# Performance work log

Hardware: AMD Instinct MI355X
Metric: run time of the kernel (lower is better)

## Reference

```python
import jax, jax.numpy as jnp
import numpy as np

B, S, D = 2, 2048, 256
H, C = 8, 32          # headNum, cDim (D == H*C)
OUT = 256             # outDim
WIN = 32              # localWindowSize (half-width)
NEG = -1e30


def setup_inputs() -> dict:
    key = jax.random.key(0)
    ks = jax.random.split(key, 9)
    scale_qk = 1.0 / np.sqrt(D)
    return {
        "Qin": jax.random.normal(ks[0], (B, S, D), jnp.float32),
        "Kin": jax.random.normal(ks[1], (B, S, D), jnp.float32),
        "Vin": jax.random.normal(ks[2], (B, S, D), jnp.float32),
        "QTrans": jax.random.normal(ks[3], (D, H * C), jnp.float32) * scale_qk,
        "KTrans": jax.random.normal(ks[4], (D, H * C), jnp.float32) * scale_qk,
        "VTrans": jax.random.normal(ks[5], (D, H * C), jnp.float32) * scale_qk,
        "GW": jax.random.normal(ks[6], (H * C, D), jnp.float32) * scale_qk,  # nn.Linear weight [out,in]
        "Gb": jnp.ones((H * C,), jnp.float32),
        "OW": jax.random.normal(ks[7], (OUT, H * C), jnp.float32) * scale_qk,
        "Ob": jnp.zeros((OUT,), jnp.float32),
    }


def reference(Qin, Kin, Vin, QTrans, KTrans, VTrans, GW, Gb, OW, Ob):
    b, s, _ = Qin.shape
    # projections -> [b, s, H, C]
    Q = (Qin @ QTrans).reshape(b, s, H, C)
    K = (Kin @ KTrans).reshape(b, s, H, C)
    V = (Vin @ VTrans).reshape(b, s, H, C)
    G = jax.nn.sigmoid(Vin @ GW.T + Gb).reshape(b, s, H, C)

    # dense scores [b, H, s, t] (matches original hnst layout with batch/head swapped)
    A = jnp.einsum('bshc,bthc->bhst', Q, K) / jnp.sqrt(jnp.asarray(C, Q.dtype))

    # whose index clamping only re-hits in-window edge positions)
    idx = jnp.arange(s)
    local = jnp.abs(idx[:, None] - idx[None, :]) <= WIN  # [s, s]
    A = jnp.where(local[None, None, :, :], A, NEG)

    A = jax.nn.softmax(A, axis=-1)

    # gated attention output: original einsum 'hnst,hnti,hnsi->nshi'
    O = jnp.einsum('bhst,bthc,bshc->bshc', A, V, G)
    return O.reshape(b, s, H * C) @ OW.T + Ob
```

## Files before the change

### kernel.cpp

```cpp
#include <hip/hip_runtime.h>
#include <hip/hip_bf16.h>

typedef __bf16 bf16_t;
typedef __attribute__((ext_vector_type(8))) __bf16 bf16x8;
typedef __attribute__((ext_vector_type(4))) __bf16 bf16x4;
typedef __attribute__((ext_vector_type(4))) float f32x4;

#define MFMA(a, b, c) __builtin_amdgcn_mfma_f32_16x16x32_bf16((a), (b), (c), 0, 0, 0)

static __device__ __forceinline__ bf16x8 zero_bf16x8() {
  bf16x8 z;
#pragma unroll
  for (int i = 0; i < 8; ++i) z[i] = (bf16_t)0.f;
  return z;
}

__global__ __launch_bounds__(256) void prep_weights(
    const float* __restrict__ QT, const float* __restrict__ KT,
    const float* __restrict__ VTr, const float* __restrict__ GW,
    const float* __restrict__ OW, bf16_t* __restrict__ Wb) {
  int e = blockIdx.x * 256 + threadIdx.x;
  int mat = e >> 16;
  int r = e & 65535;
  const float* src = (mat == 0) ? QT : (mat == 1) ? KT : (mat == 2) ? VTr
                     : (mat == 3) ? GW : OW;
  float v = src[r];
  int dst;
  if (mat < 3) {
    int k = r >> 8, n = r & 255;
    dst = n * 256 + k;
  } else {
    dst = r;
  }
  Wb[mat * 65536 + dst] = (bf16_t)v;
}

__global__ __launch_bounds__(256) void proj_kernel(
    const float* __restrict__ Qin, const float* __restrict__ Kin,
    const float* __restrict__ Vin, const bf16_t* __restrict__ Wb,
    const float* __restrict__ Gb, bf16_t* __restrict__ Qb,
    bf16_t* __restrict__ Kb, bf16_t* __restrict__ VT, bf16_t* __restrict__ G) {
  const int tid = threadIdx.x, w = tid >> 6, lane = tid & 63;
  const int quad = lane >> 4, t15 = lane & 15;
  const int job = blockIdx.z;
  const int m0 = blockIdx.x * 64 + w * 16;
  const int n0 = blockIdx.y * 64;
  const float* A = (job == 0) ? Qin : (job == 1) ? Kin : Vin;
  const bf16_t* W = Wb + job * 65536;

  const f32x4 zf = {0.f, 0.f, 0.f, 0.f};
  f32x4 acc[4] = {zf, zf, zf, zf};

  for (int kc = 0; kc < 8; ++kc) {
    const float* ap = A + (size_t)(m0 + t15) * 256 + kc * 32 + quad * 8;
    float4 x0 = *(const float4*)ap;
    float4 x1 = *(const float4*)(ap + 4);
    bf16x8 a;
    a[0] = (bf16_t)x0.x; a[1] = (bf16_t)x0.y; a[2] = (bf16_t)x0.z; a[3] = (bf16_t)x0.w;
    a[4] = (bf16_t)x1.x; a[5] = (bf16_t)x1.y; a[6] = (bf16_t)x1.z; a[7] = (bf16_t)x1.w;
#pragma unroll
    for (int nf = 0; nf < 4; ++nf) {
      bf16x8 bw = *(const bf16x8*)(W + (size_t)(n0 + nf * 16 + t15) * 256 + kc * 32 + quad * 8);
      acc[nf] = MFMA(a, bw, acc[nf]);
    }
  }

  const int mm0 = m0 + quad * 4;
  if (job == 2) {
    const int b = mm0 >> 11;
    const int s = mm0 & 2047;
#pragma unroll
    for (int nf = 0; nf < 4; ++nf) {
      int nn = n0 + nf * 16 + t15;
      int h = nn >> 5, c = nn & 31;
      bf16x4 v4;
#pragma unroll
      for (int r = 0; r < 4; ++r) v4[r] = (bf16_t)acc[nf][r];
      *(bf16x4*)(VT + (size_t)((b * 8 + h) * 32 + c) * 2048 + s) = v4;
    }
  } else if (job == 3) {
#pragma unroll
    for (int nf = 0; nf < 4; ++nf) {
      int nn = n0 + nf * 16 + t15;
      float bias = Gb[nn];
#pragma unroll
      for (int r = 0; r < 4; ++r) {
        float g = 1.f / (1.f + __expf(-(acc[nf][r] + bias)));
        G[(size_t)(mm0 + r) * 256 + nn] = (bf16_t)g;
      }
    }
  } else {
    bf16_t* dst = (job == 0) ? Qb : Kb;
#pragma unroll
    for (int nf = 0; nf < 4; ++nf) {
      int nn = n0 + nf * 16 + t15;
#pragma unroll
      for (int r = 0; r < 4; ++r)
        dst[(size_t)(mm0 + r) * 256 + nn] = (bf16_t)acc[nf][r];
    }
  }
}

__global__ __launch_bounds__(256) void attn_kernel(
    const bf16_t* __restrict__ Qb, const bf16_t* __restrict__ Kb,
    const bf16_t* __restrict__ VT, const bf16_t* __restrict__ G,
    bf16_t* __restrict__ O) {
  __shared__ bf16_t P[4][16][104];
  const int tid = threadIdx.x, w = tid >> 6, lane = tid & 63;
  const int quad = lane >> 4, t15 = lane & 15;
  const int unit = blockIdx.x * 4 + w;
  const int qt = unit & 127, bh = unit >> 7;
  const int h = bh & 7, b = bh >> 3;
  const int q0 = qt * 16, tbase = q0 - 32;
  const size_t rowbase = (size_t)b * 2048;

  bf16x8 aq = *(const bf16x8*)(Qb + (rowbase + q0 + t15) * 256 + h * 32 + quad * 8);

  const f32x4 zf = {0.f, 0.f, 0.f, 0.f};
  f32x4 sc[5];
#pragma unroll
  for (int j = 0; j < 5; ++j) {
    int t = tbase + j * 16 + t15;
    bf16x8 bk = zero_bf16x8();
    if ((unsigned)t < 2048u)
      bk = *(const bf16x8*)(Kb + (rowbase + t) * 256 + h * 32 + quad * 8);
    sc[j] = MFMA(aq, bk, zf);
  }

  const float scale = 0.17677669529663687f;
  float mx[4] = {-3.0e38f, -3.0e38f, -3.0e38f, -3.0e38f};
#pragma unroll
  for (int j = 0; j < 5; ++j) {
    int t = tbase + j * 16 + t15;
#pragma unroll
    for (int r = 0; r < 4; ++r) {
      int q = q0 + quad * 4 + r;
      int dd = q - t;
      bool valid = ((unsigned)t < 2048u) && (dd <= 32) && (dd >= -32);
      float v = valid ? sc[j][r] * scale : -1e30f;
      sc[j][r] = v;
      mx[r] = fmaxf(mx[r], v);
    }
  }
#pragma unroll
  for (int off = 1; off < 16; off <<= 1) {
#pragma unroll
    for (int r = 0; r < 4; ++r) mx[r] = fmaxf(mx[r], __shfl_xor(mx[r], off));
  }
  float sum[4] = {0.f, 0.f, 0.f, 0.f};
#pragma unroll
  for (int j = 0; j < 5; ++j) {
#pragma unroll
    for (int r = 0; r < 4; ++r) {
      float e = __expf(sc[j][r] - mx[r]);
      sc[j][r] = e;
      sum[r] += e;
    }
  }
#pragma unroll
  for (int off = 1; off < 16; off <<= 1) {
#pragma unroll
    for (int r = 0; r < 4; ++r) sum[r] += __shfl_xor(sum[r], off);
  }
  float inv[4];
#pragma unroll
  for (int r = 0; r < 4; ++r) inv[r] = 1.f / sum[r];

#pragma unroll
  for (int j = 0; j < 5; ++j) {
#pragma unroll
    for (int r = 0; r < 4; ++r)
      P[w][quad * 4 + r][j * 16 + t15] = (bf16_t)(sc[j][r] * inv[r]);
  }
#pragma unroll
  for (int r = 0; r < 4; ++r) P[w][quad * 4 + r][80 + t15] = (bf16_t)0.f;
  __syncthreads();

  f32x4 y0 = zf, y1 = zf;
#pragma unroll
  for (int kc = 0; kc < 3; ++kc) {
    bf16x8 pa = *(const bf16x8*)&P[w][t15][kc * 32 + quad * 8];
    int ts = tbase + kc * 32 + quad * 8;
    bf16x8 bv0 = zero_bf16x8(), bv1 = zero_bf16x8();
    if (ts >= 0 && ts + 8 <= 2048) {
      const bf16_t* vbase = VT + ((size_t)((b * 8 + h) * 32) + t15) * 2048 + ts;
      bv0 = *(const bf16x8*)vbase;
      bv1 = *(const bf16x8*)(vbase + (size_t)16 * 2048);
    }
    y0 = MFMA(pa, bv0, y0);
    y1 = MFMA(pa, bv1, y1);
  }

#pragma unroll
  for (int r = 0; r < 4; ++r) {
    int q = q0 + quad * 4 + r;
    size_t base = (rowbase + q) * 256 + h * 32;
    float g0 = (float)G[base + t15];
    float g1 = (float)G[base + 16 + t15];
    O[base + t15] = (bf16_t)(y0[r] * g0);
    O[base + 16 + t15] = (bf16_t)(y1[r] * g1);
  }
}

__global__ __launch_bounds__(256) void out_kernel(
    const bf16_t* __restrict__ O, const bf16_t* __restrict__ OWb,
    const float* __restrict__ Ob, float* __restrict__ out) {
  const int tid = threadIdx.x, w = tid >> 6, lane = tid & 63;
  const int quad = lane >> 4, t15 = lane & 15;
  const int m0 = blockIdx.x * 64 + w * 16;
  const int n0 = blockIdx.y * 64;

  const f32x4 zf = {0.f, 0.f, 0.f, 0.f};
  f32x4 acc[4] = {zf, zf, zf, zf};

  for (int kc = 0; kc < 8; ++kc) {
    bf16x8 a = *(const bf16x8*)(O + (size_t)(m0 + t15) * 256 + kc * 32 + quad * 8);
#pragma unroll
    for (int nf = 0; nf < 4; ++nf) {
      bf16x8 bw = *(const bf16x8*)(OWb + (size_t)(n0 + nf * 16 + t15) * 256 + kc * 32 + quad * 8);
      acc[nf] = MFMA(a, bw, acc[nf]);
    }
  }

  const int mm0 = m0 + quad * 4;
#pragma unroll
  for (int nf = 0; nf < 4; ++nf) {
    int nn = n0 + nf * 16 + t15;
    float bias = Ob[nn];
#pragma unroll
    for (int r = 0; r < 4; ++r)
      out[(size_t)(mm0 + r) * 256 + nn] = acc[nf][r] + bias;
  }
}

extern "C" void kernel_launch(void* const* d_in, const int* in_sizes, int n_in,
                              void* d_out, int out_size, void* d_ws, size_t ws_size,
                              hipStream_t stream) {
  const float* Qin = (const float*)d_in[0];
  const float* Kin = (const float*)d_in[1];
  const float* Vin = (const float*)d_in[2];
  const float* QT  = (const float*)d_in[3];
  const float* KT  = (const float*)d_in[4];
  const float* VTr = (const float*)d_in[5];
  const float* GW  = (const float*)d_in[6];
  const float* Gb  = (const float*)d_in[7];
  const float* OW  = (const float*)d_in[8];
  const float* Ob  = (const float*)d_in[9];
  float* out = (float*)d_out;

  char* ws = (char*)d_ws;
  const size_t MB = 1u << 20;
  bf16_t* Qb = (bf16_t*)(ws + 0 * MB);
  bf16_t* Kb = (bf16_t*)(ws + 2 * MB);
  bf16_t* VT = (bf16_t*)(ws + 4 * MB);
  bf16_t* G  = (bf16_t*)(ws + 6 * MB);
  bf16_t* O  = (bf16_t*)(ws + 8 * MB);
  bf16_t* Wb = (bf16_t*)(ws + 10 * MB);

  prep_weights<<<1280, 256, 0, stream>>>(QT, KT, VTr, GW, OW, Wb);
  proj_kernel<<<dim3(64, 4, 4), 256, 0, stream>>>(Qin, Kin, Vin, Wb, Gb, Qb, Kb, VT, G);
  attn_kernel<<<512, 256, 0, stream>>>(Qb, Kb, VT, G, O);
  out_kernel<<<dim3(64, 4), 256, 0, stream>>>(O, Wb + 4 * 65536, Ob, out);
}
```

Before: 116.7 us.

## Fuse weight conversion into projection and output projection into attention

Drops the separate weight-prep kernel. The projection kernel now converts its fp32 weight tile to bf16 directly into shared memory, transposing where needed. The attention kernel is widened so one 512-thread block covers all 8 heads of a 16-row query tile, keeps the gated output in LDS, and applies the output projection in place. This removes two launches and the global round trip of O and the bf16 weights, at the cost of redundant fp32 weight reads and conversion in every block and only 256 blocks for the fused attention stage.

```diff
diff --git a/kernel.cpp b/kernel.cpp
--- a/kernel.cpp
+++ b/kernel.cpp
@@ -8,6 +8,8 @@
 
 #define MFMA(a, b, c) __builtin_amdgcn_mfma_f32_16x16x32_bf16((a), (b), (c), 0, 0, 0)
 
+#define WK 260
+
 static __device__ __forceinline__ bf16x8 zero_bf16x8() {
   bf16x8 z;
 #pragma unroll
@@ -15,38 +17,63 @@
   return z;
 }
 
-__global__ __launch_bounds__(256) void prep_weights(
-    const float* __restrict__ QT, const float* __restrict__ KT,
-    const float* __restrict__ VTr, const float* __restrict__ GW,
-    const float* __restrict__ OW, bf16_t* __restrict__ Wb) {
-  int e = blockIdx.x * 256 + threadIdx.x;
-  int mat = e >> 16;
-  int r = e & 65535;
-  const float* src = (mat == 0) ? QT : (mat == 1) ? KT : (mat == 2) ? VTr
-                     : (mat == 3) ? GW : OW;
-  float v = src[r];
-  int dst;
-  if (mat < 3) {
-    int k = r >> 8, n = r & 255;
-    dst = n * 256 + k;
-  } else {
-    dst = r;
-  }
-  Wb[mat * 65536 + dst] = (bf16_t)v;
+static __device__ __forceinline__ bf16x8 join8(bf16x4 lo, bf16x4 hi) {
+  bf16x8 r;
+  r[0] = lo[0]; r[1] = lo[1]; r[2] = lo[2]; r[3] = lo[3];
+  r[4] = hi[0]; r[5] = hi[1]; r[6] = hi[2]; r[7] = hi[3];
+  return r;
+}
+
+static __device__ __forceinline__ bf16x8 cvt8(float4 a, float4 b) {
+  bf16x8 r;
+  r[0] = (bf16_t)a.x; r[1] = (bf16_t)a.y; r[2] = (bf16_t)a.z; r[3] = (bf16_t)a.w;
+  r[4] = (bf16_t)b.x; r[5] = (bf16_t)b.y; r[6] = (bf16_t)b.z; r[7] = (bf16_t)b.w;
+  return r;
 }
 
 __global__ __launch_bounds__(256) void proj_kernel(
     const float* __restrict__ Qin, const float* __restrict__ Kin,
-    const float* __restrict__ Vin, const bf16_t* __restrict__ Wb,
-    const float* __restrict__ Gb, bf16_t* __restrict__ Qb,
-    bf16_t* __restrict__ Kb, bf16_t* __restrict__ VT, bf16_t* __restrict__ G) {
+    const float* __restrict__ Vin, const float* __restrict__ QT,
+    const float* __restrict__ KT, const float* __restrict__ VTr,
+    const float* __restrict__ GW, const float* __restrict__ Gb,
+    bf16_t* __restrict__ Qb, bf16_t* __restrict__ Kb,
+    bf16_t* __restrict__ VT, bf16_t* __restrict__ G) {
+  __shared__ bf16_t Wl[64][WK];
   const int tid = threadIdx.x, w = tid >> 6, lane = tid & 63;
   const int quad = lane >> 4, t15 = lane & 15;
   const int job = blockIdx.z;
   const int m0 = blockIdx.x * 64 + w * 16;
   const int n0 = blockIdx.y * 64;
   const float* A = (job == 0) ? Qin : (job == 1) ? Kin : Vin;
-  const bf16_t* W = Wb + job * 65536;
+
+  if (job < 3) {
+    const float* src = (job == 0) ? QT : (job == 1) ? KT : VTr;
+    const int nl = tid & 63;
+    const int kq = (tid >> 6) * 4;
+#pragma unroll
+    for (int i = 0; i < 16; ++i) {
+      int k0 = i * 16 + kq;
+      float f0 = src[(size_t)(k0 + 0) * 256 + n0 + nl];
+      float f1 = src[(size_t)(k0 + 1) * 256 + n0 + nl];
+      float f2 = src[(size_t)(k0 + 2) * 256 + n0 + nl];
+      float f3 = src[(size_t)(k0 + 3) * 256 + n0 + nl];
+      bf16x4 w4;
+      w4[0] = (bf16_t)f0; w4[1] = (bf16_t)f1; w4[2] = (bf16_t)f2; w4[3] = (bf16_t)f3;
+      *(bf16x4*)&Wl[nl][k0] = w4;
+    }
+  } else {
+    const int kk = (tid & 63) * 4;
+    const int nw = tid >> 6;
+#pragma unroll
+    for (int i = 0; i < 16; ++i) {
+      int n = i * 4 + nw;
+      float4 v = *(const float4*)(GW + (size_t)(n0 + n) * 256 + kk);
+      bf16x4 w4;
+      w4[0] = (bf16_t)v.x; w4[1] = (bf16_t)v.y; w4[2] = (bf16_t)v.z; w4[3] = (bf16_t)v.w;
+      *(bf16x4*)&Wl[n][kk] = w4;
+    }
+  }
+  __syncthreads();
 
   const f32x4 zf = {0.f, 0.f, 0.f, 0.f};
   f32x4 acc[4] = {zf, zf, zf, zf};
@@ -55,13 +82,12 @@
     const float* ap = A + (size_t)(m0 + t15) * 256 + kc * 32 + quad * 8;
     float4 x0 = *(const float4*)ap;
     float4 x1 = *(const float4*)(ap + 4);
-    bf16x8 a;
-    a[0] = (bf16_t)x0.x; a[1] = (bf16_t)x0.y; a[2] = (bf16_t)x0.z; a[3] = (bf16_t)x0.w;
-    a[4] = (bf16_t)x1.x; a[5] = (bf16_t)x1.y; a[6] = (bf16_t)x1.z; a[7] = (bf16_t)x1.w;
-#pragma unroll
-    for (int nf = 0; nf < 4; ++nf) {
-      bf16x8 bw = *(const bf16x8*)(W + (size_t)(n0 + nf * 16 + t15) * 256 + kc * 32 + quad * 8);
-      acc[nf] = MFMA(a, bw, acc[nf]);
+    bf16x8 a = cvt8(x0, x1);
+#pragma unroll
+    for (int nf = 0; nf < 4; ++nf) {
+      bf16x4 lo = *(const bf16x4*)&Wl[nf * 16 + t15][kc * 32 + quad * 8];
+      bf16x4 hi = *(const bf16x4*)&Wl[nf * 16 + t15][kc * 32 + quad * 8 + 4];
+      acc[nf] = MFMA(a, join8(lo, hi), acc[nf]);
     }
   }
 
@@ -101,16 +127,16 @@
   }
 }
 
-__global__ __launch_bounds__(256) void attn_kernel(
+__global__ __launch_bounds__(512) void attn_out_kernel(
     const bf16_t* __restrict__ Qb, const bf16_t* __restrict__ Kb,
     const bf16_t* __restrict__ VT, const bf16_t* __restrict__ G,
-    bf16_t* __restrict__ O) {
-  __shared__ bf16_t P[4][16][104];
-  const int tid = threadIdx.x, w = tid >> 6, lane = tid & 63;
+    const float* __restrict__ OW, const float* __restrict__ Ob,
+    float* __restrict__ out) {
+  __shared__ bf16_t P[8][16][104];
+  __shared__ bf16_t Ol[16][WK];
+  const int tid = threadIdx.x, h = tid >> 6, lane = tid & 63;
   const int quad = lane >> 4, t15 = lane & 15;
-  const int unit = blockIdx.x * 4 + w;
-  const int qt = unit & 127, bh = unit >> 7;
-  const int h = bh & 7, b = bh >> 3;
+  const int qt = blockIdx.x & 127, b = blockIdx.x >> 7;
   const int q0 = qt * 16, tbase = q0 - 32;
   const size_t rowbase = (size_t)b * 2048;
 
@@ -170,16 +196,16 @@
   for (int j = 0; j < 5; ++j) {
 #pragma unroll
     for (int r = 0; r < 4; ++r)
-      P[w][quad * 4 + r][j * 16 + t15] = (bf16_t)(sc[j][r] * inv[r]);
-  }
-#pragma unroll
-  for (int r = 0; r < 4; ++r) P[w][quad * 4 + r][80 + t15] = (bf16_t)0.f;
+      P[h][quad * 4 + r][j * 16 + t15] = (bf16_t)(sc[j][r] * inv[r]);
+  }
+#pragma unroll
+  for (int r = 0; r < 4; ++r) P[h][quad * 4 + r][80 + t15] = (bf16_t)0.f;
   __syncthreads();
 
   f32x4 y0 = zf, y1 = zf;
 #pragma unroll
   for (int kc = 0; kc < 3; ++kc) {
-    bf16x8 pa = *(const bf16x8*)&P[w][t15][kc * 32 + quad * 8];
+    bf16x8 pa = *(const bf16x8*)&P[h][t15][kc * 32 + quad * 8];
     int ts = tbase + kc * 32 + quad * 8;
     bf16x8 bv0 = zero_bf16x8(), bv1 = zero_bf16x8();
     if (ts >= 0 && ts + 8 <= 2048) {
@@ -197,39 +223,32 @@
     size_t base = (rowbase + q) * 256 + h * 32;
     float g0 = (float)G[base + t15];
     float g1 = (float)G[base + 16 + t15];
-    O[base + t15] = (bf16_t)(y0[r] * g0);
-    O[base + 16 + t15] = (bf16_t)(y1[r] * g1);
-  }
-}
-
-__global__ __launch_bounds__(256) void out_kernel(
-    const bf16_t* __restrict__ O, const bf16_t* __restrict__ OWb,
-    const float* __restrict__ Ob, float* __restrict__ out) {
-  const int tid = threadIdx.x, w = tid >> 6, lane = tid & 63;
-  const int quad = lane >> 4, t15 = lane & 15;
-  const int m0 = blockIdx.x * 64 + w * 16;
-  const int n0 = blockIdx.y * 64;
-
-  const f32x4 zf = {0.f, 0.f, 0.f, 0.f};
-  f32x4 acc[4] = {zf, zf, zf, zf};
-
+    Ol[quad * 4 + r][h * 32 + t15] = (bf16_t)(y0[r] * g0);
+    Ol[quad * 4 + r][h * 32 + 16 + t15] = (bf16_t)(y1[r] * g1);
+  }
+  __syncthreads();
+
+  f32x4 acc[2] = {zf, zf};
   for (int kc = 0; kc < 8; ++kc) {
-    bf16x8 a = *(const bf16x8*)(O + (size_t)(m0 + t15) * 256 + kc * 32 + quad * 8);
-#pragma unroll
-    for (int nf = 0; nf < 4; ++nf) {
-      bf16x8 bw = *(const bf16x8*)(OWb + (size_t)(n0 + nf * 16 + t15) * 256 + kc * 32 + quad * 8);
-      acc[nf] = MFMA(a, bw, acc[nf]);
-    }
-  }
-
-  const int mm0 = m0 + quad * 4;
-#pragma unroll
-  for (int nf = 0; nf < 4; ++nf) {
-    int nn = n0 + nf * 16 + t15;
-    float bias = Ob[nn];
+    bf16x4 alo = *(const bf16x4*)&Ol[t15][kc * 32 + quad * 8];
+    bf16x4 ahi = *(const bf16x4*)&Ol[t15][kc * 32 + quad * 8 + 4];
+    bf16x8 a = join8(alo, ahi);
+#pragma unroll
+    for (int nf = 0; nf < 2; ++nf) {
+      int n = h * 32 + nf * 16 + t15;
+      const float* wp = OW + (size_t)n * 256 + kc * 32 + quad * 8;
+      float4 w0 = *(const float4*)wp;
+      float4 w1 = *(const float4*)(wp + 4);
+      acc[nf] = MFMA(a, cvt8(w0, w1), acc[nf]);
+    }
+  }
+#pragma unroll
+  for (int nf = 0; nf < 2; ++nf) {
+    int n = h * 32 + nf * 16 + t15;
+    float bias = Ob[n];
 #pragma unroll
     for (int r = 0; r < 4; ++r)
-      out[(size_t)(mm0 + r) * 256 + nn] = acc[nf][r] + bias;
+      out[(rowbase + q0 + quad * 4 + r) * 256 + n] = acc[nf][r] + bias;
   }
 }
 
@@ -254,11 +273,8 @@
   bf16_t* Kb = (bf16_t*)(ws + 2 * MB);
   bf16_t* VT = (bf16_t*)(ws + 4 * MB);
   bf16_t* G  = (bf16_t*)(ws + 6 * MB);
-  bf16_t* O  = (bf16_t*)(ws + 8 * MB);
-  bf16_t* Wb = (bf16_t*)(ws + 10 * MB);
-
-  prep_weights<<<1280, 256, 0, stream>>>(QT, KT, VTr, GW, OW, Wb);
-  proj_kernel<<<dim3(64, 4, 4), 256, 0, stream>>>(Qin, Kin, Vin, Wb, Gb, Qb, Kb, VT, G);
-  attn_kernel<<<512, 256, 0, stream>>>(Qb, Kb, VT, G, O);
-  out_kernel<<<dim3(64, 4), 256, 0, stream>>>(O, Wb + 4 * 65536, Ob, out);
-}
+
+  proj_kernel<<<dim3(64, 4, 4), 256, 0, stream>>>(Qin, Kin, Vin, QT, KT, VTr,
+                                                  GW, Gb, Qb, Kb, VT, G);
+  attn_out_kernel<<<256, 512, 0, stream>>>(Qb, Kb, VT, G, OW, Ob, out);
+}
```

New measurement: 104.3 us. -10.6%, faster.
